# Performance work log

Measured on AMD Instinct MI355X. Metric: run time of the kernel, lower is better.

Reference implementation:

```python
import jax, jax.numpy as jnp
import numpy as np

B, T, J, C = 8, 243, 17, 512
H = 8
HD = C // H  # 64
SCALE = HD ** -0.5


def setup_inputs() -> dict:
    key = jax.random.key(0)
    ks = jax.random.split(key, 6)
    x = jax.random.normal(ks[0], (B, T, J, C), dtype=jnp.float32)
    # external attention map, broadcast-compatible with [B,H,J,T,T]; make it row-normalized like a softmax
    am = jax.random.uniform(ks[1], (B, H, J, T, T), dtype=jnp.float32)
    att_map = am / jnp.sum(am, axis=-1, keepdims=True)
    weight = jax.random.uniform(ks[2], (1,), dtype=jnp.float32)
    w_qkv = jax.random.normal(ks[3], (3 * C, C), dtype=jnp.float32) * 0.02
    w_proj = jax.random.normal(ks[4], (C, C), dtype=jnp.float32) * 0.02
    b_proj = jax.random.normal(ks[5], (C,), dtype=jnp.float32) * 0.02
    return {"x": x, "att_map": att_map, "weight": weight,
            "w_qkv": w_qkv, "w_proj": w_proj, "b_proj": b_proj}


def reference(x, att_map, weight, w_qkv, w_proj, b_proj):
    b, t, j, c = x.shape
    h, hd = H, c // H
    # qkv projection (no bias): [B,T,J,3C] -> [3,B,H,T,J,hd]
    qkv = jnp.einsum('btjc,dc->btjd', x, w_qkv).reshape(b, t, j, 3, h, hd)
    qkv = jnp.transpose(qkv, (3, 0, 4, 1, 2, 5))
    q, k, v = qkv[0], qkv[1], qkv[2]
    # transpose T <-> J: attention runs over the temporal axis per joint
    qt = jnp.swapaxes(q, 2, 3)  # [B,H,J,T,hd]
    kt = jnp.swapaxes(k, 2, 3)
    vt = jnp.swapaxes(v, 2, 3)
    attn = jnp.einsum('bhjtc,bhjsc->bhjts', qt, kt) * SCALE  # [B,H,J,T,T]
    attn = jax.nn.softmax(attn, axis=-1)
    # blend with external attention map (dropout p=0.0 -> identity)
    attn = weight * attn + (1.0 - weight) * att_map
    out = jnp.einsum('bhjts,bhjsc->bhjtc', attn, vt)  # [B,H,J,T,hd]
    out = jnp.transpose(out, (0, 3, 2, 1, 4)).reshape(b, t, j, c)  # [B,T,J,C]
    out = out @ w_proj.T + b_proj
    return out
```

## Files before the change

kernel.cpp:

```cpp
#include <hip/hip_runtime.h>
#include <hip/hip_bf16.h>

#define B_ 8
#define T_ 243
#define J_ 17
#define C_ 512
#define H_ 8
#define HD_ 64
#define M_ (B_*T_*J_)
#define SCALE_ 0.125f
#define QKV_ELEMS (B_*H_*J_*T_*HD_)

typedef __attribute__((ext_vector_type(4))) float f32x4;
typedef __attribute__((ext_vector_type(8))) short bf16x8;

__device__ __forceinline__ ushort f2bf(float f) {
  union { float f; unsigned u; } v; v.f = f;
  unsigned r = v.u + 0x7FFFu + ((v.u >> 16) & 1u);
  return (ushort)(r >> 16);
}
__device__ __forceinline__ int vchunk(int g, int row) {
  return g ^ (row & 7) ^ ((row >> 3) & 7);
}
__device__ __forceinline__ void gll16(const void* g, void* l) {
  __builtin_amdgcn_global_load_lds(
      (__attribute__((address_space(1))) void*)g,
      (__attribute__((address_space(3))) void*)l, 16, 0, 0);
}

__global__ __launch_bounds__(256) void cvt_kernel(const float* __restrict__ in,
                                                  ushort* __restrict__ out, int n8) {
  int i = blockIdx.x * 256 + threadIdx.x;
  if (i >= n8) return;
  const float4* p = (const float4*)in + (size_t)i * 2;
  float4 v0 = p[0], v1 = p[1];
  bf16x8 o;
  o[0] = (short)f2bf(v0.x); o[1] = (short)f2bf(v0.y);
  o[2] = (short)f2bf(v0.z); o[3] = (short)f2bf(v0.w);
  o[4] = (short)f2bf(v1.x); o[5] = (short)f2bf(v1.y);
  o[6] = (short)f2bf(v1.z); o[7] = (short)f2bf(v1.w);
  *(bf16x8*)(out + (size_t)i * 8) = o;
}

template<int EPI>
__global__ __launch_bounds__(256) void gemm_bt(
    const ushort* __restrict__ A, const ushort* __restrict__ Bm,
    ushort* __restrict__ qkvout, float* __restrict__ fout,
    const float* __restrict__ bias)
{
  __shared__ alignas(16) ushort As[128 * 64];
  __shared__ alignas(16) ushort Bs[128 * 64];
  const int tid = threadIdx.x;
  const int lane = tid & 63;
  const int lo = lane & 15, hi = lane >> 4;
  const int wave = tid >> 6;
  const int wr = wave >> 1, wc = wave & 1;
  const int mt = blockIdx.x, nt = blockIdx.y;

  f32x4 acc[4][4] = {};

  for (int ks = 0; ks < 8; ++ks) {
    const int k0 = ks * 64;
    __syncthreads();
    #pragma unroll
    for (int i = 0; i < 4; ++i) {
      int c = tid + i * 256;
      int row = c >> 3;
      int col8g = (c & 7) ^ (row & 7);
      int arow = mt * 128 + row; if (arow > M_ - 1) arow = M_ - 1;
      gll16(A + (size_t)arow * 512 + k0 + col8g * 8, As + c * 8);
    }
    #pragma unroll
    for (int i = 0; i < 4; ++i) {
      int c = tid + i * 256;
      int row = c >> 3;
      int col8g = (c & 7) ^ (row & 7);
      int brow = nt * 128 + row;
      gll16(Bm + (size_t)brow * 512 + k0 + col8g * 8, Bs + c * 8);
    }
    __syncthreads();
    #pragma unroll
    for (int kk = 0; kk < 2; ++kk) {
      bf16x8 af[4], bf[4];
      #pragma unroll
      for (int mf = 0; mf < 4; ++mf) {
        int row = wr * 64 + mf * 16 + lo;
        int sc = (kk * 4 + hi) ^ (row & 7);
        af[mf] = *(const bf16x8*)(As + row * 64 + sc * 8);
      }
      #pragma unroll
      for (int nf = 0; nf < 4; ++nf) {
        int row = wc * 64 + nf * 16 + lo;
        int sc = (kk * 4 + hi) ^ (row & 7);
        bf[nf] = *(const bf16x8*)(Bs + row * 64 + sc * 8);
      }
      #pragma unroll
      for (int mf = 0; mf < 4; ++mf)
        #pragma unroll
        for (int nf = 0; nf < 4; ++nf)
          acc[mf][nf] = __builtin_amdgcn_mfma_f32_16x16x32_bf16(af[mf], bf[nf], acc[mf][nf], 0, 0, 0);
    }
  }

  if (EPI == 0) {
    const int which = nt >> 2;
    const int h = (nt * 2 + wc) & 7;
    const float scale = (which == 0) ? SCALE_ : 1.0f;
    ushort* basep = qkvout + (size_t)which * QKV_ELEMS;
    #pragma unroll
    for (int mf = 0; mf < 4; ++mf) {
      #pragma unroll
      for (int i = 0; i < 4; ++i) {
        int r = mt * 128 + wr * 64 + mf * 16 + hi * 4 + i;
        if (r >= M_) continue;
        int b = r / (T_ * J_);
        int rem = r - b * (T_ * J_);
        int t = rem / J_;
        int j = rem - t * J_;
        size_t rowoff = (((size_t)(b * H_ + h) * J_ + j) * T_ + t) * HD_;
        #pragma unroll
        for (int nf = 0; nf < 4; ++nf) {
          int hd = nf * 16 + lo;
          basep[rowoff + hd] = f2bf(acc[mf][nf][i] * scale);
        }
      }
    }
  } else {
    #pragma unroll
    for (int mf = 0; mf < 4; ++mf) {
      #pragma unroll
      for (int i = 0; i < 4; ++i) {
        int r = mt * 128 + wr * 64 + mf * 16 + hi * 4 + i;
        if (r >= M_) continue;
        #pragma unroll
        for (int nf = 0; nf < 4; ++nf) {
          int n = nt * 128 + wc * 64 + nf * 16 + lo;
          fout[(size_t)r * C_ + n] = acc[mf][nf][i] + bias[n];
        }
      }
    }
  }
}

__global__ __launch_bounds__(256, 3) void attn_kernel(
    const ushort* __restrict__ q, const ushort* __restrict__ k,
    const ushort* __restrict__ v, const float* __restrict__ am,
    const float* __restrict__ wptr, ushort* __restrict__ outO)
{
  __shared__ ushort Vt[64 * 256];
  __shared__ ushort Ps[64 * 128];
  __shared__ float red0[2][64];
  __shared__ float red1[2][64];

  const int tid = threadIdx.x;
  const int lane = tid & 63;
  const int lo = lane & 15, hi = lane >> 4;
  const int wave = tid >> 6;
  const int wr = wave >> 1, wc = wave & 1;
  const int bid = blockIdx.x;
  const int workid = (bid & 7) * 544 + (bid >> 3);
  const int bhj = workid >> 2, rt = workid & 3;
  const int bh = bhj / J_, j = bhj - bh * J_;
  const int b = bh >> 3, h = bh & 7;
  const float w = wptr[0];
  const float wb = 1.0f - w;
  const size_t kvbase = (size_t)bhj * (T_ * HD_);
  const int r0 = rt * 64;

  #pragma unroll
  for (int it = 0; it < 8; ++it) {
    int c = tid + it * 256;
    int s = c >> 3, hd0 = (c & 7) * 8;
    bf16x8 val = {};
    if (s < T_) val = *(const bf16x8*)(v + kvbase + (size_t)s * HD_ + hd0);
    #pragma unroll
    for (int e = 0; e < 8; ++e) {
      int row = hd0 + e;
      int chunk = vchunk(s >> 3, row);
      Vt[row * 256 + chunk * 8 + (s & 7)] = (ushort)val[e];
    }
  }
  __syncthreads();

  bf16x8 aq[2][2];
  #pragma unroll
  for (int mf = 0; mf < 2; ++mf) {
    int t = r0 + wr * 32 + mf * 16 + lo; if (t > T_ - 1) t = T_ - 1;
    #pragma unroll
    for (int kk = 0; kk < 2; ++kk)
      aq[mf][kk] = *(const bf16x8*)(q + kvbase + (size_t)t * HD_ + kk * 32 + hi * 8);
  }

  f32x4 acc[2][8] = {};
  __builtin_amdgcn_s_setprio(1);
  #pragma unroll
  for (int nf = 0; nf < 8; ++nf) {
    int s = wc * 128 + nf * 16 + lo; if (s > T_ - 1) s = T_ - 1;
    #pragma unroll
    for (int kk = 0; kk < 2; ++kk) {
      bf16x8 bk = *(const bf16x8*)(k + kvbase + (size_t)s * HD_ + kk * 32 + hi * 8);
      #pragma unroll
      for (int mf = 0; mf < 2; ++mf)
        acc[mf][nf] = __builtin_amdgcn_mfma_f32_16x16x32_bf16(aq[mf][kk], bk, acc[mf][nf], 0, 0, 0);
    }
  }
  __builtin_amdgcn_s_setprio(0);

  float rmax[2][4];
  #pragma unroll
  for (int mf = 0; mf < 2; ++mf)
    #pragma unroll
    for (int i = 0; i < 4; ++i) {
      float m = -1e30f;
      #pragma unroll
      for (int nf = 0; nf < 8; ++nf) {
        int s = wc * 128 + nf * 16 + lo;
        if (s < T_) m = fmaxf(m, acc[mf][nf][i]);
      }
      rmax[mf][i] = m;
    }
  #pragma unroll
  for (int d = 1; d < 16; d <<= 1)
    #pragma unroll
    for (int mf = 0; mf < 2; ++mf)
      #pragma unroll
      for (int i = 0; i < 4; ++i)
        rmax[mf][i] = fmaxf(rmax[mf][i], __shfl_xor(rmax[mf][i], d, 64));
  if (lo == 0) {
    #pragma unroll
    for (int mf = 0; mf < 2; ++mf)
      #pragma unroll
      for (int i = 0; i < 4; ++i)
        red0[wc][wr * 32 + mf * 16 + hi * 4 + i] = rmax[mf][i];
  }
  __syncthreads();

  float rsum[2][4];
  #pragma unroll
  for (int mf = 0; mf < 2; ++mf)
    #pragma unroll
    for (int i = 0; i < 4; ++i) {
      float Mx = fmaxf(rmax[mf][i], red0[wc ^ 1][wr * 32 + mf * 16 + hi * 4 + i]);
      float ssum = 0.f;
      #pragma unroll
      for (int nf = 0; nf < 8; ++nf) {
        int s = wc * 128 + nf * 16 + lo;
        float e = 0.f;
        if (s < T_) e = __expf(acc[mf][nf][i] - Mx);
        acc[mf][nf][i] = e;
        ssum += e;
      }
      rsum[mf][i] = ssum;
    }
  #pragma unroll
  for (int d = 1; d < 16; d <<= 1)
    #pragma unroll
    for (int mf = 0; mf < 2; ++mf)
      #pragma unroll
      for (int i = 0; i < 4; ++i)
        rsum[mf][i] += __shfl_xor(rsum[mf][i], d, 64);
  if (lo == 0) {
    #pragma unroll
    for (int mf = 0; mf < 2; ++mf)
      #pragma unroll
      for (int i = 0; i < 4; ++i)
        red1[wc][wr * 32 + mf * 16 + hi * 4 + i] = rsum[mf][i];
  }
  __syncthreads();

  float pinv[2][4];
  #pragma unroll
  for (int mf = 0; mf < 2; ++mf)
    #pragma unroll
    for (int i = 0; i < 4; ++i) {
      float L = rsum[mf][i] + red1[wc ^ 1][wr * 32 + mf * 16 + hi * 4 + i];
      pinv[mf][i] = w / L;
    }

  f32x4 oacc[2][2] = {};
  #pragma unroll
  for (int h2 = 0; h2 < 2; ++h2) {
    __syncthreads();
    if (wc == h2) {
      #pragma unroll
      for (int mf = 0; mf < 2; ++mf)
        #pragma unroll
        for (int i = 0; i < 4; ++i) {
          int row_local = wr * 32 + mf * 16 + hi * 4 + i;
          float pw = pinv[mf][i];
          #pragma unroll
          for (int nf = 0; nf < 8; ++nf) {
            int s = h2 * 128 + nf * 16 + lo;
            float p = (s < T_) ? acc[mf][nf][i] * pw : 0.f;
            int s_local = nf * 16 + lo;
            int chunk = (s_local >> 3) ^ (row_local & 7);
            Ps[row_local * 128 + chunk * 8 + (s_local & 7)] = f2bf(p);
          }
        }
    }
    __syncthreads();
    __builtin_amdgcn_s_setprio(1);
    #pragma unroll
    for (int kk = 0; kk < 4; ++kk) {
      bf16x8 ap[2], bv[2];
      #pragma unroll
      for (int mf = 0; mf < 2; ++mf) {
        int row = wr * 32 + mf * 16 + lo;
        int chunk = (kk * 4 + hi) ^ (row & 7);
        ap[mf] = *(const bf16x8*)(Ps + row * 128 + chunk * 8);
      }
      #pragma unroll
      for (int nf = 0; nf < 2; ++nf) {
        int row = wc * 32 + nf * 16 + lo;
        int chunk = vchunk((h2 * 4 + kk) * 4 + hi, row);
        bv[nf] = *(const bf16x8*)(Vt + row * 256 + chunk * 8);
      }
      #pragma unroll
      for (int mf = 0; mf < 2; ++mf)
        #pragma unroll
        for (int nf = 0; nf < 2; ++nf)
          oacc[mf][nf] = __builtin_amdgcn_mfma_f32_16x16x32_bf16(ap[mf], bv[nf], oacc[mf][nf], 0, 0, 0);
    }
    __builtin_amdgcn_s_setprio(0);
  }

  const float* amrow[2];
  #pragma unroll
  for (int mf = 0; mf < 2; ++mf) {
    int t = r0 + wr * 32 + mf * 16 + lo; if (t > T_ - 1) t = T_ - 1;
    amrow[mf] = am + (size_t)bhj * (T_ * T_) + (size_t)t * T_;
  }
  f32x4 amacc[2][2] = {};
  #pragma unroll
  for (int kk = 0; kk < 8; ++kk) {
    const int s8 = kk * 32 + hi * 8;
    bf16x8 aa[2];
    #pragma unroll
    for (int mf = 0; mf < 2; ++mf) {
      bf16x8 r;
      if (s8 + 7 <= T_ - 1) {
        #pragma unroll
        for (int e = 0; e < 8; ++e) r[e] = (short)f2bf(amrow[mf][s8 + e]);
      } else {
        #pragma unroll
        for (int e = 0; e < 8; ++e) {
          int s = s8 + e;
          r[e] = (s <= T_ - 1) ? (short)f2bf(amrow[mf][s]) : (short)0;
        }
      }
      aa[mf] = r;
    }
    bf16x8 bv[2];
    #pragma unroll
    for (int nf = 0; nf < 2; ++nf) {
      int row = wc * 32 + nf * 16 + lo;
      int chunk = vchunk(kk * 4 + hi, row);
      bv[nf] = *(const bf16x8*)(Vt + row * 256 + chunk * 8);
    }
    #pragma unroll
    for (int mf = 0; mf < 2; ++mf)
      #pragma unroll
      for (int nf = 0; nf < 2; ++nf)
        amacc[mf][nf] = __builtin_amdgcn_mfma_f32_16x16x32_bf16(aa[mf], bv[nf], amacc[mf][nf], 0, 0, 0);
  }

  #pragma unroll
  for (int mf = 0; mf < 2; ++mf)
    #pragma unroll
    for (int i = 0; i < 4; ++i) {
      int t = r0 + wr * 32 + mf * 16 + hi * 4 + i;
      if (t >= T_) continue;
      size_t orow = ((size_t)(b * T_ + t) * J_ + j) * C_ + h * HD_;
      #pragma unroll
      for (int nf = 0; nf < 2; ++nf) {
        int hd = wc * 32 + nf * 16 + lo;
        outO[orow + hd] = f2bf(oacc[mf][nf][i] + wb * amacc[mf][nf][i]);
      }
    }
}

extern "C" void kernel_launch(void* const* d_in, const int* in_sizes, int n_in,
                              void* d_out, int out_size, void* d_ws, size_t ws_size,
                              hipStream_t stream) {
  const float* x      = (const float*)d_in[0];
  const float* am     = (const float*)d_in[1];
  const float* weight = (const float*)d_in[2];
  const float* w_qkv  = (const float*)d_in[3];
  const float* w_proj = (const float*)d_in[4];
  const float* b_proj = (const float*)d_in[5];
  float* outp = (float*)d_out;

  char* ws = (char*)d_ws;
  ushort* wqkv_bf  = (ushort*)(ws);
  ushort* wproj_bf = (ushort*)(ws + 1572864);
  ushort* xbf      = (ushort*)(ws + 2097152);
  ushort* qws      = (ushort*)(ws + 35938304);
  ushort* kws = qws + QKV_ELEMS;
  ushort* vws = kws + QKV_ELEMS;
  if (ws_size < 137461760ull) return;

  cvt_kernel<<<8262, 256, 0, stream>>>(x, xbf, 2115072);
  cvt_kernel<<<384, 256, 0, stream>>>(w_qkv, wqkv_bf, 98304);
  cvt_kernel<<<128, 256, 0, stream>>>(w_proj, wproj_bf, 32768);

  gemm_bt<0><<<dim3(259, 12), 256, 0, stream>>>(xbf, wqkv_bf, qws, nullptr, nullptr);

  attn_kernel<<<4352, 256, 0, stream>>>(qws, kws, vws, am, weight, xbf);

  gemm_bt<1><<<dim3(259, 4), 256, 0, stream>>>(xbf, wproj_bf, nullptr, outp, b_proj);
}
```

Measured before the change: 343.8 us.

## Prefetch att_map fragments early, shrink LDS, and raise attention occupancy

The att_map rows are now loaded ahead of the softmax reductions, in two halves, so the global reads can overlap the QK^T/softmax work instead of sitting at the tail of the kernel. The P tile buffer is halved (P·V done in four phases) and the reduction scratch is aliased into it to cut LDS, while launch bounds rise to 4 blocks per CU. Float-to-bf16 conversion uses the packed v_cvt_pk_bf16_f32 instruction instead of manual rounding. The costs are more register pressure from the held fragments under a tighter register budget (risk of spills), and extra barriers from the additional P·V phases.

```diff
diff --git a/kernel.cpp b/kernel.cpp
--- a/kernel.cpp
+++ b/kernel.cpp
@@ -26,6 +26,21 @@
   __builtin_amdgcn_global_load_lds(
       (__attribute__((address_space(1))) void*)g,
       (__attribute__((address_space(3))) void*)l, 16, 0, 0);
+}
+__device__ __forceinline__ bf16x8 load_am_frag(const float* __restrict__ amrow, int s8) {
+  float fv[8];
+  if (s8 + 7 <= T_ - 1) {
+    #pragma unroll
+    for (int e = 0; e < 8; ++e) fv[e] = amrow[s8 + e];
+  } else {
+    #pragma unroll
+    for (int e = 0; e < 8; ++e) { int s = s8 + e; fv[e] = (s <= T_ - 1) ? amrow[s] : 0.f; }
+  }
+  union { bf16x8 v; unsigned u[4]; } r;
+  #pragma unroll
+  for (int p = 0; p < 4; ++p)
+    asm("v_cvt_pk_bf16_f32 %0, %1, %2" : "=v"(r.u[p]) : "v"(fv[2 * p]), "v"(fv[2 * p + 1]));
+  return r.v;
 }
 
 __global__ __launch_bounds__(256) void cvt_kernel(const float* __restrict__ in,
@@ -142,15 +157,15 @@
   }
 }
 
-__global__ __launch_bounds__(256, 3) void attn_kernel(
+__global__ __launch_bounds__(256, 4) void attn_kernel(
     const ushort* __restrict__ q, const ushort* __restrict__ k,
     const ushort* __restrict__ v, const float* __restrict__ am,
     const float* __restrict__ wptr, ushort* __restrict__ outO)
 {
   __shared__ ushort Vt[64 * 256];
-  __shared__ ushort Ps[64 * 128];
-  __shared__ float red0[2][64];
-  __shared__ float red1[2][64];
+  __shared__ alignas(16) ushort Ps[64 * 64];
+  float* red0 = (float*)Ps;
+  float* red1 = ((float*)Ps) + 128;
 
   const int tid = threadIdx.x;
   const int lane = tid & 63;
@@ -182,10 +197,17 @@
   }
   __syncthreads();
 
-  bf16x8 aq[2][2];
+  const float* amrow[2];
   #pragma unroll
   for (int mf = 0; mf < 2; ++mf) {
     int t = r0 + wr * 32 + mf * 16 + lo; if (t > T_ - 1) t = T_ - 1;
+    amrow[mf] = am + (size_t)bhj * (T_ * T_) + (size_t)t * T_;
+  }
+
+  bf16x8 aq[2][2];
+  #pragma unroll
+  for (int mf = 0; mf < 2; ++mf) {
+    int t = r0 + wr * 32 + mf * 16 + lo; if (t > T_ - 1) t = T_ - 1;
     #pragma unroll
     for (int kk = 0; kk < 2; ++kk)
       aq[mf][kk] = *(const bf16x8*)(q + kvbase + (size_t)t * HD_ + kk * 32 + hi * 8);
@@ -205,6 +227,13 @@
     }
   }
   __builtin_amdgcn_s_setprio(0);
+
+  bf16x8 aaF[2][4];
+  #pragma unroll
+  for (int kk = 0; kk < 4; ++kk)
+    #pragma unroll
+    for (int mf = 0; mf < 2; ++mf)
+      aaF[mf][kk] = load_am_frag(amrow[mf], kk * 32 + hi * 8);
 
   float rmax[2][4];
   #pragma unroll
@@ -231,7 +260,7 @@
     for (int mf = 0; mf < 2; ++mf)
       #pragma unroll
       for (int i = 0; i < 4; ++i)
-        red0[wc][wr * 32 + mf * 16 + hi * 4 + i] = rmax[mf][i];
+        red0[wc * 64 + wr * 32 + mf * 16 + hi * 4 + i] = rmax[mf][i];
   }
   __syncthreads();
 
@@ -240,7 +269,7 @@
   for (int mf = 0; mf < 2; ++mf)
     #pragma unroll
     for (int i = 0; i < 4; ++i) {
-      float Mx = fmaxf(rmax[mf][i], red0[wc ^ 1][wr * 32 + mf * 16 + hi * 4 + i]);
+      float Mx = fmaxf(rmax[mf][i], red0[(wc ^ 1) * 64 + wr * 32 + mf * 16 + hi * 4 + i]);
       float ssum = 0.f;
       #pragma unroll
       for (int nf = 0; nf < 8; ++nf) {
@@ -264,7 +293,7 @@
     for (int mf = 0; mf < 2; ++mf)
       #pragma unroll
       for (int i = 0; i < 4; ++i)
-        red1[wc][wr * 32 + mf * 16 + hi * 4 + i] = rsum[mf][i];
+        red1[wc * 64 + wr * 32 + mf * 16 + hi * 4 + i] = rsum[mf][i];
   }
   __syncthreads();
 
@@ -273,15 +302,56 @@
   for (int mf = 0; mf < 2; ++mf)
     #pragma unroll
     for (int i = 0; i < 4; ++i) {
-      float L = rsum[mf][i] + red1[wc ^ 1][wr * 32 + mf * 16 + hi * 4 + i];
+      float L = rsum[mf][i] + red1[(wc ^ 1) * 64 + wr * 32 + mf * 16 + hi * 4 + i];
       pinv[mf][i] = w / L;
     }
 
+  f32x4 amacc[2][2] = {};
+  __builtin_amdgcn_s_setprio(1);
+  #pragma unroll
+  for (int kk = 0; kk < 4; ++kk) {
+    bf16x8 bv[2];
+    #pragma unroll
+    for (int nf = 0; nf < 2; ++nf) {
+      int row = wc * 32 + nf * 16 + lo;
+      bv[nf] = *(const bf16x8*)(Vt + row * 256 + vchunk(kk * 4 + hi, row) * 8);
+    }
+    #pragma unroll
+    for (int mf = 0; mf < 2; ++mf)
+      #pragma unroll
+      for (int nf = 0; nf < 2; ++nf)
+        amacc[mf][nf] = __builtin_amdgcn_mfma_f32_16x16x32_bf16(aaF[mf][kk], bv[nf], amacc[mf][nf], 0, 0, 0);
+  }
+  __builtin_amdgcn_s_setprio(0);
+  bf16x8 aaS[2][4];
+  #pragma unroll
+  for (int kk = 0; kk < 4; ++kk)
+    #pragma unroll
+    for (int mf = 0; mf < 2; ++mf)
+      aaS[mf][kk] = load_am_frag(amrow[mf], (kk + 4) * 32 + hi * 8);
+  __builtin_amdgcn_s_setprio(1);
+  #pragma unroll
+  for (int kk = 0; kk < 4; ++kk) {
+    bf16x8 bv[2];
+    #pragma unroll
+    for (int nf = 0; nf < 2; ++nf) {
+      int row = wc * 32 + nf * 16 + lo;
+      bv[nf] = *(const bf16x8*)(Vt + row * 256 + vchunk((kk + 4) * 4 + hi, row) * 8);
+    }
+    #pragma unroll
+    for (int mf = 0; mf < 2; ++mf)
+      #pragma unroll
+      for (int nf = 0; nf < 2; ++nf)
+        amacc[mf][nf] = __builtin_amdgcn_mfma_f32_16x16x32_bf16(aaS[mf][kk], bv[nf], amacc[mf][nf], 0, 0, 0);
+  }
+  __builtin_amdgcn_s_setprio(0);
+
   f32x4 oacc[2][2] = {};
   #pragma unroll
-  for (int h2 = 0; h2 < 2; ++h2) {
+  for (int ph = 0; ph < 4; ++ph) {
     __syncthreads();
-    if (wc == h2) {
+    if (wc == (ph >> 1)) {
+      const int nfbase = (ph & 1) * 4;
       #pragma unroll
       for (int mf = 0; mf < 2; ++mf)
         #pragma unroll
@@ -289,31 +359,32 @@
           int row_local = wr * 32 + mf * 16 + hi * 4 + i;
           float pw = pinv[mf][i];
           #pragma unroll
-          for (int nf = 0; nf < 8; ++nf) {
-            int s = h2 * 128 + nf * 16 + lo;
-            float p = (s < T_) ? acc[mf][nf][i] * pw : 0.f;
+          for (int nf = 0; nf < 4; ++nf) {
+            int nfg = nfbase + nf;
+            int s = wc * 128 + nfg * 16 + lo;
+            float p = (s < T_) ? acc[mf][nfg][i] * pw : 0.f;
             int s_local = nf * 16 + lo;
             int chunk = (s_local >> 3) ^ (row_local & 7);
-            Ps[row_local * 128 + chunk * 8 + (s_local & 7)] = f2bf(p);
+            Ps[row_local * 64 + chunk * 8 + (s_local & 7)] = f2bf(p);
           }
         }
     }
     __syncthreads();
     __builtin_amdgcn_s_setprio(1);
     #pragma unroll
-    for (int kk = 0; kk < 4; ++kk) {
+    for (int kk = 0; kk < 2; ++kk) {
       bf16x8 ap[2], bv[2];
       #pragma unroll
       for (int mf = 0; mf < 2; ++mf) {
         int row = wr * 32 + mf * 16 + lo;
         int chunk = (kk * 4 + hi) ^ (row & 7);
-        ap[mf] = *(const bf16x8*)(Ps + row * 128 + chunk * 8);
+        ap[mf] = *(const bf16x8*)(Ps + row * 64 + chunk * 8);
       }
       #pragma unroll
       for (int nf = 0; nf < 2; ++nf) {
         int row = wc * 32 + nf * 16 + lo;
-        int chunk = vchunk((h2 * 4 + kk) * 4 + hi, row);
-        bv[nf] = *(const bf16x8*)(Vt + row * 256 + chunk * 8);
+        int g = ph * 8 + kk * 4 + hi;
+        bv[nf] = *(const bf16x8*)(Vt + row * 256 + vchunk(g, row) * 8);
       }
       #pragma unroll
       for (int mf = 0; mf < 2; ++mf)
@@ -322,46 +393,6 @@
           oacc[mf][nf] = __builtin_amdgcn_mfma_f32_16x16x32_bf16(ap[mf], bv[nf], oacc[mf][nf], 0, 0, 0);
     }
     __builtin_amdgcn_s_setprio(0);
-  }
-
-  const float* amrow[2];
-  #pragma unroll
-  for (int mf = 0; mf < 2; ++mf) {
-    int t = r0 + wr * 32 + mf * 16 + lo; if (t > T_ - 1) t = T_ - 1;
-    amrow[mf] = am + (size_t)bhj * (T_ * T_) + (size_t)t * T_;
-  }
-  f32x4 amacc[2][2] = {};
-  #pragma unroll
-  for (int kk = 0; kk < 8; ++kk) {
-    const int s8 = kk * 32 + hi * 8;
-    bf16x8 aa[2];
-    #pragma unroll
-    for (int mf = 0; mf < 2; ++mf) {
-      bf16x8 r;
-      if (s8 + 7 <= T_ - 1) {
-        #pragma unroll
-        for (int e = 0; e < 8; ++e) r[e] = (short)f2bf(amrow[mf][s8 + e]);
-      } else {
-        #pragma unroll
-        for (int e = 0; e < 8; ++e) {
-          int s = s8 + e;
-          r[e] = (s <= T_ - 1) ? (short)f2bf(amrow[mf][s]) : (short)0;
-        }
-      }
-      aa[mf] = r;
-    }
-    bf16x8 bv[2];
-    #pragma unroll
-    for (int nf = 0; nf < 2; ++nf) {
-      int row = wc * 32 + nf * 16 + lo;
-      int chunk = vchunk(kk * 4 + hi, row);
-      bv[nf] = *(const bf16x8*)(Vt + row * 256 + chunk * 8);
-    }
-    #pragma unroll
-    for (int mf = 0; mf < 2; ++mf)
-      #pragma unroll
-      for (int nf = 0; nf < 2; ++nf)
-        amacc[mf][nf] = __builtin_amdgcn_mfma_f32_16x16x32_bf16(aa[mf], bv[nf], amacc[mf][nf], 0, 0, 0);
   }
 
   #pragma unroll
```

Result: slower. 477.2 us (+38.8%).
